# Performance work log

Hardware: AMD Instinct MI355X
Metric: run time of the kernel (lower is better)

## Reference

```python
import jax, jax.numpy as jnp
import numpy as np
from jax import lax


def _lstm_dir(x, w_ih, w_hh, b_ih, b_hh, reverse):
    """Single-direction LSTM over x: [B, S, D]. PyTorch gate order i,f,g,o.
    Returns hidden sequence [B, S, H], aligned with input time order."""
    B, S, _ = x.shape
    H = w_hh.shape[1]
    # Fuse input projection across all timesteps: [B, S, 4H]
    xg = jnp.einsum('bsd,gd->bsg', x, w_ih) + b_ih + b_hh
    h0 = jnp.zeros((B, H), x.dtype)
    c0 = jnp.zeros((B, H), x.dtype)

    def step(carry, xg_t):
        h, c = carry
        g = xg_t + h @ w_hh.T  # [B, 4H]
        i, f, gg, o = jnp.split(g, 4, axis=-1)
        i = jax.nn.sigmoid(i)
        f = jax.nn.sigmoid(f)
        gg = jnp.tanh(gg)
        o = jax.nn.sigmoid(o)
        c = f * c + i * gg
        h = o * jnp.tanh(c)
        return (h, c), h

    (hT, cT), hs = lax.scan(step, (h0, c0), jnp.swapaxes(xg, 0, 1), reverse=reverse)
    return jnp.swapaxes(hs, 0, 1), hT, cT  # hs: [B, S, H]


def _bilstm(x, layers):
    out = x
    for (wif, whf, bif, bhf, wib, whb, bib, bhb) in layers:
        hf, _, _ = _lstm_dir(out, wif, whf, bif, bhf, reverse=False)
        hb, _, _ = _lstm_dir(out, wib, whb, bib, bhb, reverse=True)
        out = jnp.concatenate([hf, hb], axis=-1)
    return out


def setup_inputs() -> dict:
    key = jax.random.key(0)
    B, S, D, H, O, L = 64, 512, 256, 512, 128, 2
    ks = jax.random.split(key, 32)
    ki = iter(range(32))
    s = 1.0 / np.sqrt(H)

    def u(shape):
        return jax.random.uniform(ks[next(ki)], shape, jnp.float32, -s, s)

    inp = {"x": jax.random.normal(ks[next(ki)], (B, S, D), jnp.float32)}
    for l in range(L):
        din = D if l == 0 else 2 * H
        for d in ('f', 'b'):
            inp[f"w_ih_l{l}_{d}"] = u((4 * H, din))
            inp[f"w_hh_l{l}_{d}"] = u((4 * H, H))
            inp[f"b_ih_l{l}_{d}"] = u((4 * H,))
            inp[f"b_hh_l{l}_{d}"] = u((4 * H,))
    inp["fc_w"] = u((O, 2 * H))
    inp["fc_b"] = u((O,))
    return inp


def reference(x,
              w_ih_l0_f, w_hh_l0_f, b_ih_l0_f, b_hh_l0_f,
              w_ih_l0_b, w_hh_l0_b, b_ih_l0_b, b_hh_l0_b,
              w_ih_l1_f, w_hh_l1_f, b_ih_l1_f, b_hh_l1_f,
              w_ih_l1_b, w_hh_l1_b, b_ih_l1_b, b_hh_l1_b,
              fc_w, fc_b):
    layers = [
        (w_ih_l0_f, w_hh_l0_f, b_ih_l0_f, b_hh_l0_f,
         w_ih_l0_b, w_hh_l0_b, b_ih_l0_b, b_hh_l0_b),
        (w_ih_l1_f, w_hh_l1_f, b_ih_l1_f, b_hh_l1_f,
         w_ih_l1_b, w_hh_l1_b, b_ih_l1_b, b_hh_l1_b),
    ]
    out = _bilstm(x, layers)          # [B, S, 2H]
    last = out[:, -1, :]               # [B, 2H]
    return last @ fc_w.T + fc_b        # [B, O]
```

## Files before the change

kernel.cpp:

```cpp
#include <hip/hip_runtime.h>
#include <math.h>

#define Bn 64
#define Sn 512
#define Dn 256
#define Hn 512
#define On 128

using short8 = __attribute__((ext_vector_type(8))) short;
using f32x4  = __attribute__((ext_vector_type(4))) float;

union U8 { unsigned u[4]; short8 s; };

__device__ __forceinline__ ushort f2bf(float f) {
    unsigned u = __float_as_uint(f);
    u = u + 0x7FFFu + ((u >> 16) & 1u);
    return (ushort)(u >> 16);
}
__device__ __forceinline__ float bf2f(ushort b) {
    return __uint_as_float(((unsigned)b) << 16);
}
__device__ __forceinline__ void split8(const float* __restrict__ p, short8& hi, short8& lo) {
    #pragma unroll
    for (int j = 0; j < 8; ++j) {
        float w = p[j];
        ushort h = f2bf(w);
        hi[j] = (short)h;
        lo[j] = (short)f2bf(w - bf2f(h));
    }
}
__device__ __forceinline__ void pin8(short8& v) { asm volatile("" : "+v"(v)); }

__device__ __forceinline__ void lda8(const unsigned* p, unsigned* w) {
    const unsigned long long* q = (const unsigned long long*)p;
    #pragma unroll
    for (int j = 0; j < 4; ++j) {
        unsigned long long v = __hip_atomic_load(q + j, __ATOMIC_RELAXED, __HIP_MEMORY_SCOPE_AGENT);
        w[2*j]   = (unsigned)v;
        w[2*j+1] = (unsigned)(v >> 32);
    }
}
__device__ __forceinline__ void unpack8(const unsigned* w, short8& hi8, short8& lo8) {
    U8 a, b;
    #pragma unroll
    for (int j = 0; j < 4; ++j) {
        a.u[j] = (w[2*j] & 0xffffu) | (w[2*j+1] << 16);
        b.u[j] = (w[2*j] >> 16)     | (w[2*j+1] & 0xffff0000u);
    }
    hi8 = a.s; lo8 = b.s;
}
__device__ __forceinline__ void sta32(unsigned* p, unsigned v) {
    __hip_atomic_store(p, v, __ATOMIC_RELAXED, __HIP_MEMORY_SCOPE_AGENT);
}

__device__ __forceinline__ void poll_ge(const unsigned* p, unsigned epoch) {
    while (__hip_atomic_load(p, __ATOMIC_RELAXED, __HIP_MEMORY_SCOPE_AGENT) < epoch)
        __builtin_amdgcn_s_sleep(1);
}
__device__ __forceinline__ void wait_group(const unsigned* base, int n, unsigned epoch) {
    if ((int)threadIdx.x < n)
        poll_ge(base + threadIdx.x, epoch);
    __syncthreads();
}
__device__ __forceinline__ void publish_slot(unsigned* slot, unsigned epoch) {
    __syncthreads();
    if (threadIdx.x == 0)
        __hip_atomic_store(slot, epoch, __ATOMIC_RELAXED, __HIP_MEMORY_SCOPE_AGENT);
}

__device__ __forceinline__ f32x4 mfma_bf16(short8 a, short8 b, f32x4 c) {
    return __builtin_amdgcn_mfma_f32_16x16x32_bf16(a, b, c, 0, 0, 0);
}

__global__ __launch_bounds__(256, 1) void bilstm_persistent(
    const float* __restrict__ x,
    const float* __restrict__ wih0f, const float* __restrict__ whh0f,
    const float* __restrict__ bih0f, const float* __restrict__ bhh0f,
    const float* __restrict__ wih0b, const float* __restrict__ whh0b,
    const float* __restrict__ bih0b, const float* __restrict__ bhh0b,
    const float* __restrict__ wih1f, const float* __restrict__ whh1f,
    const float* __restrict__ bih1f, const float* __restrict__ bhh1f,
    const float* __restrict__ wih1b, const float* __restrict__ whh1b,
    const float* __restrict__ bih1b, const float* __restrict__ bhh1b,
    const float* __restrict__ fcw,  const float* __restrict__ fcb,
    unsigned* flags,
    unsigned* h0_pk,
    unsigned* h1_pk,
    unsigned* h1b_pk,
    unsigned* out0_pk,
    float* out)
{
    const int bid = blockIdx.x;
    const int tid = threadIdx.x;
    const int l  = tid & 63;
    const int w  = tid >> 6;
    const int lc = l & 15;
    const int ks = l >> 4;

    __shared__ float P[4 * 4 * 16 * 20];
    __shared__ short8 wl[6144];
    __shared__ float hstage[2][Hn];

    {
        const int dir = bid >> 7;
        const int hs  = (bid >> 2) & 31;
        const int bt  = bid & 3;
        unsigned* g1 = &flags[(dir * 4 + bt) * 32];
        const float* wih = dir ? wih0b : wih0f;
        const float* whh = dir ? whh0b : whh0f;
        const float* bih = dir ? bih0b : bih0f;
        const float* bhh = dir ? bhh0b : bhh0f;

        short8 wh_hi[4][4];
        #pragma unroll
        for (int i = 0; i < 4; ++i) {
            const int k0 = (w * 4 + i) * 32 + ks * 8;
            #pragma unroll
            for (int nt = 0; nt < 4; ++nt) {
                const int r = nt * 512 + hs * 16 + lc;
                short8 hi, lo;
                split8(&whh[(size_t)r * 512 + k0], hi, lo);
                wh_hi[i][nt] = hi;
                wl[(w * 16 + i * 4 + nt) * 64 + l] = lo;
            }
        }
        short8 wx_hi[2][4];
        #pragma unroll
        for (int i = 0; i < 2; ++i) {
            const int k0 = (w * 2 + i) * 32 + ks * 8;
            #pragma unroll
            for (int nt = 0; nt < 4; ++nt) {
                const int r = nt * 512 + hs * 16 + lc;
                short8 hi, lo;
                split8(&wih[(size_t)r * 256 + k0], hi, lo);
                wx_hi[i][nt] = hi;
                wl[4096 + (w * 8 + i * 4 + nt) * 64 + l] = lo;
            }
        }
        #pragma unroll
        for (int i = 0; i < 4; ++i)
            #pragma unroll
            for (int nt = 0; nt < 4; ++nt) pin8(wh_hi[i][nt]);
        #pragma unroll
        for (int i = 0; i < 2; ++i)
            #pragma unroll
            for (int nt = 0; nt < 4; ++nt) pin8(wx_hi[i][nt]);
        const short8* whlo = &wl[(w * 16) * 64 + l];
        const short8* wxlo = &wl[4096 + (w * 8) * 64 + l];

        const int cb = bt * 16 + (tid >> 4);
        const int ch = hs * 16 + (tid & 15);
        float bias_r[4];
        #pragma unroll
        for (int gt = 0; gt < 4; ++gt)
            bias_r[gt] = bih[gt * 512 + ch] + bhh[gt * 512 + ch];
        float c_reg = 0.f;
        const int bA = bt * 16 + lc;

        f32x4 xg0 = {0.f,0.f,0.f,0.f}, xg1 = xg0, xg2 = xg0, xg3 = xg0;
        {
            const int tt = dir ? (Sn - 1) : 0;
            #pragma unroll
            for (int i = 0; i < 2; ++i) {
                const int k0 = (w * 2 + i) * 32 + ks * 8;
                short8 xh, xl;
                split8(&x[((size_t)bA * Sn + tt) * Dn + k0], xh, xl);
                xg0 = mfma_bf16(xh, wx_hi[i][0], xg0); xg0 = mfma_bf16(xl, wx_hi[i][0], xg0); xg0 = mfma_bf16(xh, wxlo[(i*4+0)*64], xg0);
                xg1 = mfma_bf16(xh, wx_hi[i][1], xg1); xg1 = mfma_bf16(xl, wx_hi[i][1], xg1); xg1 = mfma_bf16(xh, wxlo[(i*4+1)*64], xg1);
                xg2 = mfma_bf16(xh, wx_hi[i][2], xg2); xg2 = mfma_bf16(xl, wx_hi[i][2], xg2); xg2 = mfma_bf16(xh, wxlo[(i*4+2)*64], xg2);
                xg3 = mfma_bf16(xh, wx_hi[i][3], xg3); xg3 = mfma_bf16(xl, wx_hi[i][3], xg3); xg3 = mfma_bf16(xh, wxlo[(i*4+3)*64], xg3);
            }
        }

        for (int s = 0; s < Sn; ++s) {
            if (s) wait_group(g1, 32, (unsigned)s);

            const int p = s & 1;
            const int t = dir ? (Sn - 1 - s) : s;

            unsigned hw[4][8];
            #pragma unroll
            for (int i = 0; i < 4; ++i)
                lda8(&h0_pk[(((size_t)p * 2 + dir) * Bn + bA) * Hn + (w * 4 + i) * 32 + ks * 8], hw[i]);

            f32x4 acc0 = xg0, acc1 = xg1, acc2 = xg2, acc3 = xg3;
            #pragma unroll
            for (int i = 0; i < 4; ++i) {
                short8 ah, al;
                unpack8(hw[i], ah, al);
                acc0 = mfma_bf16(ah, wh_hi[i][0], acc0); acc0 = mfma_bf16(al, wh_hi[i][0], acc0); acc0 = mfma_bf16(ah, whlo[(i*4+0)*64], acc0);
                acc1 = mfma_bf16(ah, wh_hi[i][1], acc1); acc1 = mfma_bf16(al, wh_hi[i][1], acc1); acc1 = mfma_bf16(ah, whlo[(i*4+1)*64], acc1);
                acc2 = mfma_bf16(ah, wh_hi[i][2], acc2); acc2 = mfma_bf16(al, wh_hi[i][2], acc2); acc2 = mfma_bf16(ah, whlo[(i*4+2)*64], acc2);
                acc3 = mfma_bf16(ah, wh_hi[i][3], acc3); acc3 = mfma_bf16(al, wh_hi[i][3], acc3); acc3 = mfma_bf16(ah, whlo[(i*4+3)*64], acc3);
            }
            *(f32x4*)&P[((w * 4 + 0) * 16 + lc) * 20 + ks * 4] = acc0;
            *(f32x4*)&P[((w * 4 + 1) * 16 + lc) * 20 + ks * 4] = acc1;
            *(f32x4*)&P[((w * 4 + 2) * 16 + lc) * 20 + ks * 4] = acc2;
            *(f32x4*)&P[((w * 4 + 3) * 16 + lc) * 20 + ks * 4] = acc3;
            __syncthreads();

            unsigned word;
            {
                float g4[4];
                #pragma unroll
                for (int gt = 0; gt < 4; ++gt) {
                    float sum = bias_r[gt];
                    #pragma unroll
                    for (int ww = 0; ww < 4; ++ww)
                        sum += P[((ww * 4 + gt) * 16 + (tid & 15)) * 20 + (tid >> 4)];
                    g4[gt] = sum;
                }
                const float ig = 1.f / (1.f + expf(-g4[0]));
                const float fg = 1.f / (1.f + expf(-g4[1]));
                const float gg = tanhf(g4[2]);
                const float og = 1.f / (1.f + expf(-g4[3]));
                c_reg = fg * c_reg + ig * gg;
                const float h = og * tanhf(c_reg);
                const ushort hhv = f2bf(h);
                const ushort hlv = f2bf(h - bf2f(hhv));
                word = (unsigned)hhv | ((unsigned)hlv << 16);
                sta32(&h0_pk[(((size_t)(p ^ 1) * 2 + dir) * Bn + cb) * Hn + ch], word);
            }
            if (s == Sn - 1)
                sta32(&out0_pk[((size_t)cb * Sn + t) * 1024 + dir * 512 + ch], word);

            publish_slot(&g1[hs], (unsigned)(s + 1));

            if (s < Sn - 1) {
                sta32(&out0_pk[((size_t)cb * Sn + t) * 1024 + dir * 512 + ch], word);
                const int tt = dir ? (Sn - 2 - s) : (s + 1);
                xg0 = {0.f,0.f,0.f,0.f}; xg1 = xg0; xg2 = xg0; xg3 = xg0;
                #pragma unroll
                for (int i = 0; i < 2; ++i) {
                    const int k0 = (w * 2 + i) * 32 + ks * 8;
                    short8 xh, xl;
                    split8(&x[((size_t)bA * Sn + tt) * Dn + k0], xh, xl);
                    xg0 = mfma_bf16(xh, wx_hi[i][0], xg0); xg0 = mfma_bf16(xl, wx_hi[i][0], xg0); xg0 = mfma_bf16(xh, wxlo[(i*4+0)*64], xg0);
                    xg1 = mfma_bf16(xh, wx_hi[i][1], xg1); xg1 = mfma_bf16(xl, wx_hi[i][1], xg1); xg1 = mfma_bf16(xh, wxlo[(i*4+1)*64], xg1);
                    xg2 = mfma_bf16(xh, wx_hi[i][2], xg2); xg2 = mfma_bf16(xl, wx_hi[i][2], xg2); xg2 = mfma_bf16(xh, wxlo[(i*4+2)*64], xg2);
                    xg3 = mfma_bf16(xh, wx_hi[i][3], xg3); xg3 = mfma_bf16(xl, wx_hi[i][3], xg3); xg3 = mfma_bf16(xh, wxlo[(i*4+3)*64], xg3);
                }
            }
        }
    }

    {
        const int hs = (bid >> 2) & 63;
        const int bt = bid & 3;
        unsigned* g2 = &flags[256 + bt * 64];

        short8 wh_hi2[4][2];
        #pragma unroll
        for (int i = 0; i < 4; ++i) {
            const int k0 = (w * 4 + i) * 32 + ks * 8;
            #pragma unroll
            for (int nt = 0; nt < 2; ++nt) {
                const int c = nt * 16 + lc;
                const int r = (c >> 3) * 512 + hs * 8 + (c & 7);
                short8 hi, lo;
                split8(&whh1f[(size_t)r * 512 + k0], hi, lo);
                wh_hi2[i][nt] = hi;
                wl[(w * 8 + i * 2 + nt) * 64 + l] = lo;
            }
        }
        short8 wx_hi2[8][2];
        #pragma unroll
        for (int i = 0; i < 8; ++i) {
            const int k0 = (w * 8 + i) * 32 + ks * 8;
            #pragma unroll
            for (int nt = 0; nt < 2; ++nt) {
                const int c = nt * 16 + lc;
                const int r = (c >> 3) * 512 + hs * 8 + (c & 7);
                short8 hi, lo;
                split8(&wih1f[(size_t)r * 1024 + k0], hi, lo);
                wx_hi2[i][nt] = hi;
                wl[2048 + (w * 16 + i * 2 + nt) * 64 + l] = lo;
            }
        }
        #pragma unroll
        for (int i = 0; i < 4; ++i)
            #pragma unroll
            for (int nt = 0; nt < 2; ++nt) pin8(wh_hi2[i][nt]);
        #pragma unroll
        for (int i = 0; i < 8; ++i)
            #pragma unroll
            for (int nt = 0; nt < 2; ++nt) pin8(wx_hi2[i][nt]);
        const short8* whlo2 = &wl[(w * 8) * 64 + l];
        const short8* wxlo2 = &wl[2048 + (w * 16) * 64 + l];

        const bool is_cell = (tid < 128);
        const int cb = bt * 16 + (tid >> 3);
        const int ch = hs * 8 + (tid & 7);
        float bias_r[4] = {0.f, 0.f, 0.f, 0.f};
        if (is_cell) {
            #pragma unroll
            for (int gt = 0; gt < 4; ++gt)
                bias_r[gt] = bih1f[gt * 512 + ch] + bhh1f[gt * 512 + ch];
        }
        float c_reg = 0.f;
        const int bA = bt * 16 + lc;

        if (tid < 64)
            poll_ge(&flags[(tid >> 5) * 128 + bt * 32 + (tid & 31)], (unsigned)Sn);
        __syncthreads();

        f32x4 xg0 = {0.f,0.f,0.f,0.f}, xg1 = xg0;
        {
            unsigned ow[8][8];
            #pragma unroll
            for (int i = 0; i < 8; ++i)
                lda8(&out0_pk[(size_t)bA * Sn * 1024 + (w * 8 + i) * 32 + ks * 8], ow[i]);
            #pragma unroll
            for (int i = 0; i < 8; ++i) {
                short8 ah, al;
                unpack8(ow[i], ah, al);
                xg0 = mfma_bf16(ah, wx_hi2[i][0], xg0); xg0 = mfma_bf16(al, wx_hi2[i][0], xg0); xg0 = mfma_bf16(ah, wxlo2[(i*2+0)*64], xg0);
                xg1 = mfma_bf16(ah, wx_hi2[i][1], xg1); xg1 = mfma_bf16(al, wx_hi2[i][1], xg1); xg1 = mfma_bf16(ah, wxlo2[(i*2+1)*64], xg1);
            }
        }

        for (int s = 0; s < Sn; ++s) {
            if (s) wait_group(g2, 64, (unsigned)s);

            const int p = s & 1;
            unsigned hw[4][8];
            #pragma unroll
            for (int i = 0; i < 4; ++i)
                lda8(&h1_pk[((size_t)p * Bn + bA) * Hn + (w * 4 + i) * 32 + ks * 8], hw[i]);

            f32x4 acc0 = xg0, acc1 = xg1;
            #pragma unroll
            for (int i = 0; i < 4; ++i) {
                short8 ah, al;
                unpack8(hw[i], ah, al);
                acc0 = mfma_bf16(ah, wh_hi2[i][0], acc0); acc0 = mfma_bf16(al, wh_hi2[i][0], acc0); acc0 = mfma_bf16(ah, whlo2[(i*2+0)*64], acc0);
                acc1 = mfma_bf16(ah, wh_hi2[i][1], acc1); acc1 = mfma_bf16(al, wh_hi2[i][1], acc1); acc1 = mfma_bf16(ah, whlo2[(i*2+1)*64], acc1);
            }
            *(f32x4*)&P[((w * 2 + 0) * 16 + lc) * 20 + ks * 4] = acc0;
            *(f32x4*)&P[((w * 2 + 1) * 16 + lc) * 20 + ks * 4] = acc1;
            __syncthreads();

            if (is_cell) {
                float g4[4];
                #pragma unroll
                for (int gt = 0; gt < 4; ++gt) {
                    const int cc = gt * 8 + (tid & 7);
                    const int nt = cc >> 4, g = cc & 15;
                    float sum = bias_r[gt];
                    #pragma unroll
                    for (int ww = 0; ww < 4; ++ww)
                        sum += P[((ww * 2 + nt) * 16 + g) * 20 + (tid >> 3)];
                    g4[gt] = sum;
                }
                const float ig = 1.f / (1.f + expf(-g4[0]));
                const float fg = 1.f / (1.f + expf(-g4[1]));
                const float gg = tanhf(g4[2]);
                const float og = 1.f / (1.f + expf(-g4[3]));
                c_reg = fg * c_reg + ig * gg;
                const float h = og * tanhf(c_reg);
                const ushort hhv = f2bf(h);
                const ushort hlv = f2bf(h - bf2f(hhv));
                const unsigned word = (unsigned)hhv | ((unsigned)hlv << 16);
                sta32(&h1_pk[((size_t)(p ^ 1) * Bn + cb) * Hn + ch], word);
            }
            publish_slot(&g2[bid >> 2], (unsigned)(s + 1));

            if (s < Sn - 1) {
                unsigned ow[8][8];
                #pragma unroll
                for (int i = 0; i < 8; ++i)
                    lda8(&out0_pk[((size_t)bA * Sn + (s + 1)) * 1024 + (w * 8 + i) * 32 + ks * 8], ow[i]);
                xg0 = {0.f,0.f,0.f,0.f}; xg1 = xg0;
                #pragma unroll
                for (int i = 0; i < 8; ++i) {
                    short8 ah, al;
                    unpack8(ow[i], ah, al);
                    xg0 = mfma_bf16(ah, wx_hi2[i][0], xg0); xg0 = mfma_bf16(al, wx_hi2[i][0], xg0); xg0 = mfma_bf16(ah, wxlo2[(i*2+0)*64], xg0);
                    xg1 = mfma_bf16(ah, wx_hi2[i][1], xg1); xg1 = mfma_bf16(al, wx_hi2[i][1], xg1); xg1 = mfma_bf16(ah, wxlo2[(i*2+1)*64], xg1);
                }
            }
        }
    }

    {
        const int hs = (bid >> 2) & 63;
        const int bt = bid & 3;
        const int bA = bt * 16 + lc;
        const int t = Sn - 1;
        unsigned hw[8][8];
        #pragma unroll
        for (int i = 0; i < 8; ++i) {
            const int k0 = (w * 8 + i) * 32 + ks * 8;
            lda8(&out0_pk[((size_t)bA * Sn + t) * 1024 + k0], hw[i]);
        }
        f32x4 acc0 = {0.f,0.f,0.f,0.f}, acc1 = acc0;
        #pragma unroll
        for (int i = 0; i < 8; ++i) {
            const int k0 = (w * 8 + i) * 32 + ks * 8;
            short8 ah, al;
            unpack8(hw[i], ah, al);
            #pragma unroll
            for (int nt = 0; nt < 2; ++nt) {
                const int c = nt * 16 + lc;
                const int r = (c >> 3) * 512 + hs * 8 + (c & 7);
                short8 bh, bl;
                split8(&wih1b[(size_t)r * 1024 + k0], bh, bl);
                f32x4 a = (nt == 0) ? acc0 : acc1;
                a = mfma_bf16(ah, bh, a);
                a = mfma_bf16(al, bh, a);
                a = mfma_bf16(ah, bl, a);
                if (nt == 0) acc0 = a; else acc1 = a;
            }
        }
        *(f32x4*)&P[((w * 2 + 0) * 16 + lc) * 20 + ks * 4] = acc0;
        *(f32x4*)&P[((w * 2 + 1) * 16 + lc) * 20 + ks * 4] = acc1;
        __syncthreads();
        if (tid < 128) {
            const int cb = bt * 16 + (tid >> 3);
            const int ch = hs * 8 + (tid & 7);
            float g4[4];
            #pragma unroll
            for (int gt = 0; gt < 4; ++gt) {
                const int cc = gt * 8 + (tid & 7);
                const int nt = cc >> 4, g = cc & 15;
                float sum = bih1b[gt * 512 + ch] + bhh1b[gt * 512 + ch];
                #pragma unroll
                for (int ww = 0; ww < 4; ++ww)
                    sum += P[((ww * 2 + nt) * 16 + g) * 20 + (tid >> 3)];
                g4[gt] = sum;
            }
            const float ig = 1.f / (1.f + expf(-g4[0]));
            const float gg = tanhf(g4[2]);
            const float og = 1.f / (1.f + expf(-g4[3]));
            const float c = ig * gg;
            const float h = og * tanhf(c);
            const ushort hhv = f2bf(h);
            const ushort hlv = f2bf(h - bf2f(hhv));
            sta32(&h1b_pk[(size_t)cb * Hn + ch], (unsigned)hhv | ((unsigned)hlv << 16));
        }
        publish_slot(&flags[512 + bid], 1u);
    }

    if (bid < Bn) {
        if (tid < 256) poll_ge(&flags[512 + tid], 1u);
        __syncthreads();
        {
            const unsigned long long* qf =
                (const unsigned long long*)&h1_pk[(size_t)0 * Bn * Hn + (size_t)bid * Hn];
            const unsigned long long* qb =
                (const unsigned long long*)&h1b_pk[(size_t)bid * Hn];
            unsigned long long vf = __hip_atomic_load(qf + tid, __ATOMIC_RELAXED, __HIP_MEMORY_SCOPE_AGENT);
            unsigned long long vb = __hip_atomic_load(qb + tid, __ATOMIC_RELAXED, __HIP_MEMORY_SCOPE_AGENT);
            const int j = tid * 2;
            hstage[0][j]     = bf2f((ushort)(vf & 0xffff))         + bf2f((ushort)((vf >> 16) & 0xffff));
            hstage[0][j + 1] = bf2f((ushort)((vf >> 32) & 0xffff)) + bf2f((ushort)((vf >> 48) & 0xffff));
            hstage[1][j]     = bf2f((ushort)(vb & 0xffff))         + bf2f((ushort)((vb >> 16) & 0xffff));
            hstage[1][j + 1] = bf2f((ushort)((vb >> 32) & 0xffff)) + bf2f((ushort)((vb >> 48) & 0xffff));
        }
        __syncthreads();
        if (tid < On) {
            const int b = bid, o = tid;
            float sum = fcb[o];
            const float* wrow = &fcw[(size_t)o * 1024];
            #pragma unroll 4
            for (int j = 0; j < Hn; ++j) sum += hstage[0][j] * wrow[j];
            #pragma unroll 4
            for (int j = 0; j < Hn; ++j) sum += hstage[1][j] * wrow[512 + j];
            out[(size_t)b * On + o] = sum;
        }
    }
}

extern "C" void kernel_launch(void* const* d_in, const int* in_sizes, int n_in,
                              void* d_out, int out_size, void* d_ws, size_t ws_size,
                              hipStream_t stream)
{
    const float* x     = (const float*)d_in[0];
    const float* wih0f = (const float*)d_in[1];
    const float* whh0f = (const float*)d_in[2];
    const float* bih0f = (const float*)d_in[3];
    const float* bhh0f = (const float*)d_in[4];
    const float* wih0b = (const float*)d_in[5];
    const float* whh0b = (const float*)d_in[6];
    const float* bih0b = (const float*)d_in[7];
    const float* bhh0b = (const float*)d_in[8];
    const float* wih1f = (const float*)d_in[9];
    const float* whh1f = (const float*)d_in[10];
    const float* bih1f = (const float*)d_in[11];
    const float* bhh1f = (const float*)d_in[12];
    const float* wih1b = (const float*)d_in[13];
    const float* whh1b = (const float*)d_in[14];
    const float* bih1b = (const float*)d_in[15];
    const float* bhh1b = (const float*)d_in[16];
    const float* fcw   = (const float*)d_in[17];
    const float* fcb   = (const float*)d_in[18];

    char* ws = (char*)d_ws;
    size_t off = 0;
    unsigned* flags  = (unsigned*)(ws + off); off += (size_t)768 * 4;
    unsigned* h0_pk  = (unsigned*)(ws + off); off += (size_t)2 * 2 * Bn * Hn * 4;
    unsigned* h1_pk  = (unsigned*)(ws + off); off += (size_t)2 * Bn * Hn * 4;
    size_t zero_end = off;
    unsigned* h1b_pk = (unsigned*)(ws + off); off += (size_t)Bn * Hn * 4;
    unsigned* out0_pk = (unsigned*)(ws + off); off += (size_t)Bn * Sn * 2 * Hn * 4;

    hipMemsetAsync(d_ws, 0, zero_end, stream);

    hipLaunchKernelGGL(bilstm_persistent, dim3(256), dim3(256), 0, stream,
        x, wih0f, whh0f, bih0f, bhh0f, wih0b, whh0b, bih0b, bhh0b,
        wih1f, whh1f, bih1f, bhh1f, wih1b, whh1b, bih1b, bhh1b,
        fcw, fcb,
        flags, h0_pk, h1_pk, h1b_pk, out0_pk,
        (float*)d_out);
}
```

Before: 6.160 ms.

## Replace per-step flag barriers with epoch-tagged hidden-state words

Every hidden-state word now carries the producing step number in the upper 32 bits of a 64-bit atomic store. Consumers spin on the exact words they need rather than polling a group of per-block flags and then doing a separate load. This removes the publish syncthreads and flag-store round trip and the separate flag-wait phase from every recurrent step. In exchange, hidden-state traffic doubles in size, and each polling thread must repeatedly reload eight 64-bit words until all tags match.

```diff
diff --git a/kernel.cpp b/kernel.cpp
--- a/kernel.cpp
+++ b/kernel.cpp
@@ -9,6 +9,7 @@
 
 using short8 = __attribute__((ext_vector_type(8))) short;
 using f32x4  = __attribute__((ext_vector_type(4))) float;
+typedef unsigned long long u64;
 
 union U8 { unsigned u[4]; short8 s; };
 
@@ -32,10 +33,10 @@
 __device__ __forceinline__ void pin8(short8& v) { asm volatile("" : "+v"(v)); }
 
 __device__ __forceinline__ void lda8(const unsigned* p, unsigned* w) {
-    const unsigned long long* q = (const unsigned long long*)p;
+    const u64* q = (const u64*)p;
     #pragma unroll
     for (int j = 0; j < 4; ++j) {
-        unsigned long long v = __hip_atomic_load(q + j, __ATOMIC_RELAXED, __HIP_MEMORY_SCOPE_AGENT);
+        u64 v = __hip_atomic_load(q + j, __ATOMIC_RELAXED, __HIP_MEMORY_SCOPE_AGENT);
         w[2*j]   = (unsigned)v;
         w[2*j+1] = (unsigned)(v >> 32);
     }
@@ -53,19 +54,28 @@
     __hip_atomic_store(p, v, __ATOMIC_RELAXED, __HIP_MEMORY_SCOPE_AGENT);
 }
 
+__device__ __forceinline__ void poll8(const u64* q, unsigned tag, unsigned* w) {
+    u64 v[8];
+    for (;;) {
+        #pragma unroll
+        for (int j = 0; j < 8; ++j)
+            v[j] = __hip_atomic_load(q + j, __ATOMIC_RELAXED, __HIP_MEMORY_SCOPE_AGENT);
+        bool ok = true;
+        #pragma unroll
+        for (int j = 0; j < 8; ++j) ok &= ((unsigned)(v[j] >> 32) == tag);
+        if (ok) break;
+        __builtin_amdgcn_s_sleep(1);
+    }
+    #pragma unroll
+    for (int j = 0; j < 8; ++j) w[j] = (unsigned)v[j];
+}
+__device__ __forceinline__ void st_tag(u64* p, unsigned word, unsigned tag) {
+    __hip_atomic_store(p, (u64)word | ((u64)tag << 32), __ATOMIC_RELAXED, __HIP_MEMORY_SCOPE_AGENT);
+}
+
 __device__ __forceinline__ void poll_ge(const unsigned* p, unsigned epoch) {
     while (__hip_atomic_load(p, __ATOMIC_RELAXED, __HIP_MEMORY_SCOPE_AGENT) < epoch)
         __builtin_amdgcn_s_sleep(1);
-}
-__device__ __forceinline__ void wait_group(const unsigned* base, int n, unsigned epoch) {
-    if ((int)threadIdx.x < n)
-        poll_ge(base + threadIdx.x, epoch);
-    __syncthreads();
-}
-__device__ __forceinline__ void publish_slot(unsigned* slot, unsigned epoch) {
-    __syncthreads();
-    if (threadIdx.x == 0)
-        __hip_atomic_store(slot, epoch, __ATOMIC_RELAXED, __HIP_MEMORY_SCOPE_AGENT);
 }
 
 __device__ __forceinline__ f32x4 mfma_bf16(short8 a, short8 b, f32x4 c) {
@@ -84,8 +94,8 @@
     const float* __restrict__ bih1b, const float* __restrict__ bhh1b,
     const float* __restrict__ fcw,  const float* __restrict__ fcb,
     unsigned* flags,
-    unsigned* h0_pk,
-    unsigned* h1_pk,
+    u64* h0_tg,
+    u64* h1_tg,
     unsigned* h1b_pk,
     unsigned* out0_pk,
     float* out)
@@ -105,7 +115,7 @@
         const int dir = bid >> 7;
         const int hs  = (bid >> 2) & 31;
         const int bt  = bid & 3;
-        unsigned* g1 = &flags[(dir * 4 + bt) * 32];
+        unsigned* g1slot = &flags[(dir * 4 + bt) * 32 + hs];
         const float* wih = dir ? wih0b : wih0f;
         const float* whh = dir ? whh0b : whh0f;
         const float* bih = dir ? bih0b : bih0f;
@@ -173,15 +183,14 @@
         }
 
         for (int s = 0; s < Sn; ++s) {
-            if (s) wait_group(g1, 32, (unsigned)s);
-
             const int p = s & 1;
             const int t = dir ? (Sn - 1 - s) : s;
 
             unsigned hw[4][8];
             #pragma unroll
             for (int i = 0; i < 4; ++i)
-                lda8(&h0_pk[(((size_t)p * 2 + dir) * Bn + bA) * Hn + (w * 4 + i) * 32 + ks * 8], hw[i]);
+                poll8(&h0_tg[(((size_t)p * 2 + dir) * Bn + bA) * Hn + (w * 4 + i) * 32 + ks * 8],
+                      (unsigned)s, hw[i]);
 
             f32x4 acc0 = xg0, acc1 = xg1, acc2 = xg2, acc3 = xg3;
             #pragma unroll
@@ -219,12 +228,15 @@
                 const ushort hhv = f2bf(h);
                 const ushort hlv = f2bf(h - bf2f(hhv));
                 word = (unsigned)hhv | ((unsigned)hlv << 16);
-                sta32(&h0_pk[(((size_t)(p ^ 1) * 2 + dir) * Bn + cb) * Hn + ch], word);
+                st_tag(&h0_tg[(((size_t)((s + 1) & 1) * 2 + dir) * Bn + cb) * Hn + ch],
+                       word, (unsigned)(s + 1));
             }
             if (s == Sn - 1)
                 sta32(&out0_pk[((size_t)cb * Sn + t) * 1024 + dir * 512 + ch], word);
 
-            publish_slot(&g1[hs], (unsigned)(s + 1));
+            __syncthreads();
+            if (s == Sn - 1 && tid == 0)
+                __hip_atomic_store(g1slot, (unsigned)Sn, __ATOMIC_RELAXED, __HIP_MEMORY_SCOPE_AGENT);
 
             if (s < Sn - 1) {
                 sta32(&out0_pk[((size_t)cb * Sn + t) * 1024 + dir * 512 + ch], word);
@@ -247,7 +259,6 @@
     {
         const int hs = (bid >> 2) & 63;
         const int bt = bid & 3;
-        unsigned* g2 = &flags[256 + bt * 64];
 
         short8 wh_hi2[4][2];
         #pragma unroll
@@ -320,13 +331,13 @@
         }
 
         for (int s = 0; s < Sn; ++s) {
-            if (s) wait_group(g2, 64, (unsigned)s);
-
             const int p = s & 1;
+
             unsigned hw[4][8];
             #pragma unroll
             for (int i = 0; i < 4; ++i)
-                lda8(&h1_pk[((size_t)p * Bn + bA) * Hn + (w * 4 + i) * 32 + ks * 8], hw[i]);
+                poll8(&h1_tg[((size_t)p * Bn + bA) * Hn + (w * 4 + i) * 32 + ks * 8],
+                      (unsigned)s, hw[i]);
 
             f32x4 acc0 = xg0, acc1 = xg1;
             #pragma unroll
@@ -361,9 +372,10 @@
                 const ushort hhv = f2bf(h);
                 const ushort hlv = f2bf(h - bf2f(hhv));
                 const unsigned word = (unsigned)hhv | ((unsigned)hlv << 16);
-                sta32(&h1_pk[((size_t)(p ^ 1) * Bn + cb) * Hn + ch], word);
-            }
-            publish_slot(&g2[bid >> 2], (unsigned)(s + 1));
+                st_tag(&h1_tg[((size_t)((s + 1) & 1) * Bn + cb) * Hn + ch],
+                       word, (unsigned)(s + 1));
+            }
+            __syncthreads();
 
             if (s < Sn - 1) {
                 unsigned ow[8][8];
@@ -438,24 +450,25 @@
             const ushort hlv = f2bf(h - bf2f(hhv));
             sta32(&h1b_pk[(size_t)cb * Hn + ch], (unsigned)hhv | ((unsigned)hlv << 16));
         }
-        publish_slot(&flags[512 + bid], 1u);
+        __syncthreads();
+        if (tid == 0)
+            __hip_atomic_store(&flags[512 + bid], 1u, __ATOMIC_RELAXED, __HIP_MEMORY_SCOPE_AGENT);
     }
 
     if (bid < Bn) {
         if (tid < 256) poll_ge(&flags[512 + tid], 1u);
         __syncthreads();
         {
-            const unsigned long long* qf =
-                (const unsigned long long*)&h1_pk[(size_t)0 * Bn * Hn + (size_t)bid * Hn];
-            const unsigned long long* qb =
-                (const unsigned long long*)&h1b_pk[(size_t)bid * Hn];
-            unsigned long long vf = __hip_atomic_load(qf + tid, __ATOMIC_RELAXED, __HIP_MEMORY_SCOPE_AGENT);
-            unsigned long long vb = __hip_atomic_load(qb + tid, __ATOMIC_RELAXED, __HIP_MEMORY_SCOPE_AGENT);
-            const int j = tid * 2;
-            hstage[0][j]     = bf2f((ushort)(vf & 0xffff))         + bf2f((ushort)((vf >> 16) & 0xffff));
-            hstage[0][j + 1] = bf2f((ushort)((vf >> 32) & 0xffff)) + bf2f((ushort)((vf >> 48) & 0xffff));
-            hstage[1][j]     = bf2f((ushort)(vb & 0xffff))         + bf2f((ushort)((vb >> 16) & 0xffff));
-            hstage[1][j + 1] = bf2f((ushort)((vb >> 32) & 0xffff)) + bf2f((ushort)((vb >> 48) & 0xffff));
+            const u64* qf = &h1_tg[(size_t)0 * Bn * Hn + (size_t)bid * Hn];
+            u64 vf0 = __hip_atomic_load(qf + 2 * tid,     __ATOMIC_RELAXED, __HIP_MEMORY_SCOPE_AGENT);
+            u64 vf1 = __hip_atomic_load(qf + 2 * tid + 1, __ATOMIC_RELAXED, __HIP_MEMORY_SCOPE_AGENT);
+            const unsigned w0 = (unsigned)vf0, w1 = (unsigned)vf1;
+            hstage[0][2 * tid]     = bf2f((ushort)(w0 & 0xffff)) + bf2f((ushort)(w0 >> 16));
+            hstage[0][2 * tid + 1] = bf2f((ushort)(w1 & 0xffff)) + bf2f((ushort)(w1 >> 16));
+            const u64* qb = (const u64*)&h1b_pk[(size_t)bid * Hn];
+            u64 vb = __hip_atomic_load(qb + tid, __ATOMIC_RELAXED, __HIP_MEMORY_SCOPE_AGENT);
+            hstage[1][2 * tid]     = bf2f((ushort)(vb & 0xffff))         + bf2f((ushort)((vb >> 16) & 0xffff));
+            hstage[1][2 * tid + 1] = bf2f((ushort)((vb >> 32) & 0xffff)) + bf2f((ushort)((vb >> 48) & 0xffff));
         }
         __syncthreads();
         if (tid < On) {
@@ -497,9 +510,9 @@
 
     char* ws = (char*)d_ws;
     size_t off = 0;
-    unsigned* flags  = (unsigned*)(ws + off); off += (size_t)768 * 4;
-    unsigned* h0_pk  = (unsigned*)(ws + off); off += (size_t)2 * 2 * Bn * Hn * 4;
-    unsigned* h1_pk  = (unsigned*)(ws + off); off += (size_t)2 * Bn * Hn * 4;
+    unsigned* flags = (unsigned*)(ws + off); off += (size_t)768 * 4;
+    u64* h0_tg = (u64*)(ws + off); off += (size_t)2 * 2 * Bn * Hn * 8;
+    u64* h1_tg = (u64*)(ws + off); off += (size_t)2 * Bn * Hn * 8;
     size_t zero_end = off;
     unsigned* h1b_pk = (unsigned*)(ws + off); off += (size_t)Bn * Hn * 4;
     unsigned* out0_pk = (unsigned*)(ws + off); off += (size_t)Bn * Sn * 2 * Hn * 4;
@@ -510,6 +523,6 @@
         x, wih0f, whh0f, bih0f, bhh0f, wih0b, whh0b, bih0b, bhh0b,
         wih1f, whh1f, bih1f, bhh1f, wih1b, whh1b, bih1b, bhh1b,
         fcw, fcb,
-        flags, h0_pk, h1_pk, h1b_pk, out0_pk,
+        flags, h0_tg, h1_tg, h1b_pk, out0_pk,
         (float*)d_out);
 }
```

Result: slower. 8.581 ms (+39.3%).
